# Optimization experiments

Measured on AMD Instinct MI355X. Metric: run time of the kernel, lower is better.

## Reference

```python
import jax, jax.numpy as jnp
import numpy as np

B, N, C = 8, 3136, 128
NUM_HEADS = 2
HEAD_DIM = C // NUM_HEADS  # 64
SCALE = HEAD_DIM ** -0.5


def setup_inputs() -> dict:
    key = jax.random.key(0)
    ks = jax.random.split(key, 10)
    s = 0.02
    return {
        "x": jax.random.normal(ks[0], (B, N, C), jnp.float32),
        "H": 56,
        "W": 56,
        "relative_pos": jax.random.normal(ks[1], (NUM_HEADS, N, N), jnp.float32),
        "Wq": jax.random.normal(ks[2], (C, C), jnp.float32) * s,
        "bq": jnp.zeros((C,), jnp.float32),
        "Wk": jax.random.normal(ks[3], (C, C), jnp.float32) * s,
        "bk": jnp.zeros((C,), jnp.float32),
        "Wv": jax.random.normal(ks[4], (C, C), jnp.float32) * s,
        "bv": jnp.zeros((C,), jnp.float32),
        "Wp": jax.random.normal(ks[5], (C, C), jnp.float32) * s,
        "bp": jnp.zeros((C,), jnp.float32),
    }


def reference(x, H, W, relative_pos, Wq, bq, Wk, bk, Wv, bv, Wp, bp):
    # x: [B, N, C]; sr_ratio == 1 path of Attention.forward
    b, n, c = x.shape
    h, dh = NUM_HEADS, HEAD_DIM
    # q/k/v projections -> [B, h, N, dh] (torch Linear: x @ W.T + b)
    q = (x @ Wq.T + bq).reshape(b, n, h, dh).transpose(0, 2, 1, 3)
    k = (x @ Wk.T + bk).reshape(b, n, h, dh).transpose(0, 2, 1, 3)
    v = (x @ Wv.T + bv).reshape(b, n, h, dh).transpose(0, 2, 1, 3)
    # scores with additive relative-position bias: [B, h, N, N]
    attn = jnp.einsum("bhnd,bhmd->bhnm", q, k) * SCALE + relative_pos[None]
    attn = jax.nn.softmax(attn, axis=-1)
    # AV -> [B, N, C]
    out = jnp.einsum("bhnm,bhmd->bhnd", attn, v).transpose(0, 2, 1, 3).reshape(b, n, c)
    return out @ Wp.T + bp
```

## Files before the change

### kernel.cpp

```cpp
#include <hip/hip_runtime.h>
#include <hip/hip_fp16.h>

#define N_TOK 3136
#define DH 64
#define NHEAD 2
#define CDIM 128
#define BATCH 8
#define NT 49
#define QK_SCALE 0.18033688011112f
#define LOG2E 1.4426950408889634f

typedef __attribute__((ext_vector_type(8))) short bf16x8;
typedef __attribute__((ext_vector_type(8))) _Float16 f16x8;
typedef __attribute__((ext_vector_type(2))) _Float16 f16x2;
typedef __attribute__((ext_vector_type(2))) __fp16 fp16x2;
typedef __attribute__((ext_vector_type(4))) float f32x4;
typedef __attribute__((ext_vector_type(16))) float f32x16;
typedef __attribute__((ext_vector_type(4))) unsigned short u16x4;
typedef __attribute__((ext_vector_type(4))) unsigned int u32x4;

__device__ __forceinline__ unsigned short f2bf(float f) {
  unsigned int u = __float_as_uint(f);
  u += 0x7fffu + ((u >> 16) & 1u);
  return (unsigned short)(u >> 16);
}

#define MFMA16(a, b, c)    __builtin_amdgcn_mfma_f32_16x16x32_bf16(a, b, c, 0, 0, 0)
#define MFMA32_BF(a, b, c) __builtin_amdgcn_mfma_f32_32x32x16_bf16(a, b, c, 0, 0, 0)
#define MFMA32_F16(a, b, c) __builtin_amdgcn_mfma_f32_32x32x16_f16(a, b, c, 0, 0, 0)

__device__ __forceinline__ void plswap(unsigned& a, unsigned& b) {
  asm volatile("v_permlane32_swap_b32 %0, %1" : "+v"(a), "+v"(b));
}

__device__ __forceinline__ f16x2 pkrtz(float a, float b) {
  union { fp16x2 p; f16x2 h; } cv;
  cv.p = __builtin_amdgcn_cvt_pkrtz(a, b);
  return cv.h;
}

__device__ __forceinline__ float dot2acc(f16x2 pr, float acc) {
#if __has_builtin(__builtin_amdgcn_fdot2)
  union { f16x2 h; fp16x2 p; } c; c.h = pr;
  fp16x2 ones = {(__fp16)1.0f, (__fp16)1.0f};
  return __builtin_amdgcn_fdot2(c.p, ones, acc, false);
#else
  return acc + (float)pr[0] + (float)pr[1];
#endif
}

__device__ __forceinline__ void stage_w(const float* __restrict__ W,
                                        unsigned short (*wsh)[136], int tid) {
  const float4* Wv4 = (const float4*)W;
#pragma unroll
  for (int i = 0; i < 16; ++i) {
    int f = tid + i * 256;
    float4 v = Wv4[f];
    int row = f >> 5, col = (f & 31) << 2;
    u16x4 pk = { f2bf(v.x), f2bf(v.y), f2bf(v.z), f2bf(v.w) };
    *(u16x4*)&wsh[row][col] = pk;
  }
}

__device__ __forceinline__ void mfma_block(const unsigned short (*xs)[136],
                                           const unsigned short (*wsh)[136],
                                           int w, int lk, int lg, f32x4* acc) {
#pragma unroll
  for (int nf = 0; nf < 8; ++nf) acc[nf] = (f32x4){0.f, 0.f, 0.f, 0.f};
#pragma unroll
  for (int kk = 0; kk < 4; ++kk) {
    bf16x8 a = *(const bf16x8*)&xs[w * 16 + lk][kk * 32 + 8 * lg];
#pragma unroll
    for (int nf = 0; nf < 8; ++nf) {
      bf16x8 b = *(const bf16x8*)&wsh[nf * 16 + lk][kk * 32 + 8 * lg];
      acc[nf] = MFMA16(a, b, acc[nf]);
    }
  }
}

__global__ __launch_bounds__(256)
void proj_qkv(const float* __restrict__ x,
              const float* __restrict__ Wq, const float* __restrict__ bq,
              const float* __restrict__ Wk, const float* __restrict__ bk,
              const float* __restrict__ Wv, const float* __restrict__ bv,
              unsigned short* __restrict__ qo, unsigned short* __restrict__ ko,
              unsigned short* __restrict__ vo)
{
  __shared__ __align__(16) unsigned short xs[64][136];
  __shared__ __align__(16) unsigned short wsh[128][136];
  const int tid = threadIdx.x;
  const int m0 = blockIdx.x * 64;
  const int w = tid >> 6, l = tid & 63;
  const int lk = l & 15, lg = l >> 4;

  {
    const float4* Xv = (const float4*)(x + (size_t)m0 * CDIM);
#pragma unroll
    for (int i = 0; i < 8; ++i) {
      int f = tid + i * 256;
      float4 v = Xv[f];
      int row = f >> 5, col = (f & 31) << 2;
      u16x4 pk = { f2bf(v.x), f2bf(v.y), f2bf(v.z), f2bf(v.w) };
      *(u16x4*)&xs[row][col] = pk;
    }
  }
  stage_w(Wq, wsh, tid);
  __syncthreads();

  f32x4 acc[8];

  mfma_block(xs, wsh, w, lk, lg, acc);
#pragma unroll
  for (int reg = 0; reg < 4; ++reg) {
    int row = m0 + w * 16 + 4 * lg + reg;
    int bb = row / N_TOK, tok = row - bb * N_TOK;
#pragma unroll
    for (int nf = 0; nf < 8; ++nf) {
      int col = nf * 16 + lk;
      float val = (acc[nf][reg] + bq[col]) * QK_SCALE;
      qo[((size_t)(bb * NHEAD + (nf >> 2)) * N_TOK + tok) * DH + (col & 63)] = f2bf(val);
    }
  }
  __syncthreads();

  stage_w(Wk, wsh, tid);
  __syncthreads();
  mfma_block(xs, wsh, w, lk, lg, acc);
#pragma unroll
  for (int reg = 0; reg < 4; ++reg) {
    int row = m0 + w * 16 + 4 * lg + reg;
    int bb = row / N_TOK, tok = row - bb * N_TOK;
#pragma unroll
    for (int nf = 0; nf < 8; ++nf) {
      int col = nf * 16 + lk;
      float val = acc[nf][reg] + bk[col];
      ko[((size_t)(bb * NHEAD + (nf >> 2)) * N_TOK + tok) * DH + (col & 63)] = f2bf(val);
    }
  }
  __syncthreads();

  stage_w(Wv, wsh, tid);
  __syncthreads();
  mfma_block(xs, wsh, w, lk, lg, acc);
#pragma unroll
  for (int reg = 0; reg < 4; ++reg) {
    int row = m0 + w * 16 + 4 * lg + reg;
    int bb = row / N_TOK, tok = row - bb * N_TOK;
#pragma unroll
    for (int nf = 0; nf < 8; ++nf) {
      int col = nf * 16 + lk;
      float val = acc[nf][reg] + bv[col];
      size_t idx = ((size_t)(bb * NHEAD + (nf >> 2)) * DH + (col & 63)) * N_TOK + tok;
      vo[idx] = __half_as_ushort(__float2half(val));
    }
  }
}

__global__ __launch_bounds__(256)
void exp_rp(const float* __restrict__ rp, __half* __restrict__ E)
{
  const int hkt = blockIdx.x;
  const int h = hkt / NT, kt = hkt % NT;
  const int q0 = blockIdx.y * 64;
  const int t = threadIdx.x;
  const int kp = t & 63;
  const int qi = t >> 6;

  const int ct = kp >> 5;
  const int kpp = kp & 31;
  const int hi = (kpp >> 2) & 1;
  const int r = (kpp & 3) + ((kpp >> 3) << 2);
  const int didx = hi * 32 + ct * 16 + r;

  const float* src = rp + ((size_t)h * N_TOK + q0) * N_TOK + kt * 64 + kp;
  __half* dst = E + (((size_t)h * NT + kt) * N_TOK + q0) * 64 + didx;

#pragma unroll
  for (int i = 0; i < 16; ++i) {
    int q = qi * 16 + i;
    float v = __expf(src[(size_t)q * N_TOK]);
    dst[(size_t)q * 64] = __float2half(v);
  }
}

__global__ __launch_bounds__(256)
void attn32(const unsigned short* __restrict__ q_ws,
            const unsigned short* __restrict__ k_ws,
            const unsigned short* __restrict__ v_ws,
            const __half* __restrict__ E,
            unsigned short* __restrict__ attn_out)
{
  __shared__ __align__(16) unsigned short LDSU[2][9216];

  const int b = blockIdx.x, qt = blockIdx.y, head = blockIdx.z;
  const int tid = threadIdx.x;
  const int w = tid >> 6, l = tid & 63;
  const int lq = l & 31, hi = l >> 5;

  const size_t bh = ((size_t)b * NHEAD + head) * N_TOK;
  const unsigned short* Kp = k_ws + bh * DH;
  const _Float16* Vt = (const _Float16*)v_ws + bh * DH;

  int qg = qt * 128 + w * 32 + lq;
  if (qg > N_TOK - 1) qg = N_TOK - 1;

  bf16x8 qf[4];
  {
    const unsigned short* qrow = q_ws + (bh + (size_t)qg) * DH + 8 * hi;
#pragma unroll
    for (int ks = 0; ks < 4; ++ks) qf[ks] = *(const bf16x8*)(qrow + 16 * ks);
  }

  const int kr0 = tid >> 3, ku = tid & 7;
  const int kofs = kr0 * 72 + ku * 8;
  const int gk0 = kr0 * DH + ku * 8, gk1 = gk0 + 32 * DH;
  const int gvt0 = kr0 * N_TOK + ku * 8, gvt1 = gvt0 + 32 * N_TOK;

  const __half* Eb = E + (((size_t)head * NT) * N_TOK + (size_t)qg) * DH + hi * 32;

  float lsum = 0.f;
  f32x16 o0, o1;
#pragma unroll
  for (int i = 0; i < 16; ++i) { o0[i] = 0.f; o1[i] = 0.f; }

  bf16x8 kpreA = *(const bf16x8*)(Kp + gk0);
  bf16x8 kpreB = *(const bf16x8*)(Kp + gk1);
  f16x8 vpreA = *(const f16x8*)(Vt + gvt0);
  f16x8 vpreB = *(const f16x8*)(Vt + gvt1);

  u32x4 EwA[4], EwB[4];
  {
    const u32x4* ep = (const u32x4*)Eb;
#pragma unroll
    for (int f = 0; f < 4; ++f) EwA[f] = ep[f];
  }

  *(bf16x8*)&LDSU[0][kofs] = kpreA;
  *(bf16x8*)&LDSU[0][kofs + 32 * 72] = kpreB;
  *(f16x8*)&LDSU[0][4608 + kofs] = vpreA;
  *(f16x8*)&LDSU[0][4608 + kofs + 32 * 72] = vpreB;
  {
    const unsigned short* kn = Kp + (size_t)64 * DH;
    const _Float16* vn = Vt + 64;
    kpreA = *(const bf16x8*)(kn + gk0);
    kpreB = *(const bf16x8*)(kn + gk1);
    vpreA = *(const f16x8*)(vn + gvt0);
    vpreB = *(const f16x8*)(vn + gvt1);
  }
  asm volatile("s_waitcnt lgkmcnt(0)" ::: "memory");
  __builtin_amdgcn_s_barrier();
  asm volatile("" ::: "memory");

#define ATTN_BODY(PH, KT, EW_CUR, EW_NXT, LAST)                               \
  {                                                                           \
    const unsigned short* Kb = &LDSU[PH][0];                                  \
    const unsigned short* Vb = &LDSU[PH][4608];                               \
    unsigned short* Kn = &LDSU[PH ^ 1][0];                                    \
    unsigned short* Vn = &LDSU[PH ^ 1][4608];                                 \
    if (!(LAST)) {                                         \
      const u32x4* ep = (const u32x4*)(Eb + (size_t)((KT) + 1) * (N_TOK * DH)); \
      _Pragma("unroll") for (int f = 0; f < 4; ++f) EW_NXT[f] = ep[f];        \
    }                                                                         \
                                                           \
    f32x16 s0, s1;                                                            \
    _Pragma("unroll") for (int i = 0; i < 16; ++i) { s0[i] = 0.f; s1[i] = 0.f; } \
    __builtin_amdgcn_s_setprio(1);                                            \
    _Pragma("unroll") for (int ks = 0; ks < 4; ++ks) {                        \
      bf16x8 kf0 = *(const bf16x8*)&Kb[lq * 72 + 16 * ks + 8 * hi];           \
      s0 = MFMA32_BF(kf0, qf[ks], s0);                                        \
      bf16x8 kf1 = *(const bf16x8*)&Kb[(32 + lq) * 72 + 16 * ks + 8 * hi];    \
      s1 = MFMA32_BF(kf1, qf[ks], s1);                                        \
    }                                                                         \
    __builtin_amdgcn_s_setprio(0);                                            \
    if (!(LAST)) {            \
      *(bf16x8*)&Kn[kofs] = kpreA;                                            \
      *(bf16x8*)&Kn[kofs + 32 * 72] = kpreB;                                  \
      *(f16x8*)&Vn[kofs] = vpreA;                                             \
      *(f16x8*)&Vn[kofs + 32 * 72] = vpreB;                                   \
      if ((KT) + 2 < NT) {                                                    \
        const unsigned short* kn2 = Kp + (size_t)((KT) + 2) * 64 * DH;        \
        const _Float16* vn2 = Vt + (size_t)((KT) + 2) * 64;                   \
        kpreA = *(const bf16x8*)(kn2 + gk0);                                  \
        kpreB = *(const bf16x8*)(kn2 + gk1);                                  \
        vpreA = *(const f16x8*)(vn2 + gvt0);                                  \
        vpreB = *(const f16x8*)(vn2 + gvt1);                                  \
      }                                                                       \
    }                                                                         \
                                \
    unsigned pw[16];                                                          \
    _Pragma("unroll") for (int f = 0; f < 4; ++f) {                           \
      int rb = (f & 1) * 8;                                                   \
      _Pragma("unroll") for (int i = 0; i < 4; ++i) {                         \
        float a = (f >> 1) ? s1[rb + 2 * i] : s0[rb + 2 * i];                 \
        float c = (f >> 1) ? s1[rb + 2 * i + 1] : s0[rb + 2 * i + 1];         \
        f16x2 pp = pkrtz(__builtin_amdgcn_exp2f(a), __builtin_amdgcn_exp2f(c)); \
        union { unsigned u; f16x2 h; } ec; ec.u = EW_CUR[f][i];               \
        f16x2 pr = pp * ec.h;                                                 \
        lsum = dot2acc(pr, lsum);                                             \
        union { f16x2 h; unsigned u; } pu; pu.h = pr;                         \
        pw[4 * f + i] = pu.u;                                                 \
      }                                                                       \
      plswap(pw[4 * f + 0], pw[4 * f + 2]);                                   \
      plswap(pw[4 * f + 1], pw[4 * f + 3]);                                   \
    }                                                                         \
                                                        \
    __builtin_amdgcn_s_setprio(1);                                            \
    _Pragma("unroll") for (int ks = 0; ks < 4; ++ks) {                        \
      union { unsigned u[4]; f16x8 v; } pf;                                   \
      _Pragma("unroll") for (int i = 0; i < 4; ++i) pf.u[i] = pw[4 * ks + i]; \
      f16x8 vf0 = *(const f16x8*)&Vb[lq * 72 + 16 * ks + 8 * hi];             \
      o0 = MFMA32_F16(vf0, pf.v, o0);                                         \
      f16x8 vf1 = *(const f16x8*)&Vb[(32 + lq) * 72 + 16 * ks + 8 * hi];      \
      o1 = MFMA32_F16(vf1, pf.v, o1);                                         \
    }                                                                         \
    __builtin_amdgcn_s_setprio(0);                                            \
    if (!(LAST)) {                                                            \
      asm volatile("s_waitcnt lgkmcnt(0)" ::: "memory");                      \
      __builtin_amdgcn_s_barrier();                                           \
      asm volatile("" ::: "memory");                                          \
    }                                                                         \
  }

  for (int kt2 = 0; kt2 < (NT - 1) / 2; ++kt2) {
    int kt = 2 * kt2;
    ATTN_BODY(0, kt, EwA, EwB, false);
    ATTN_BODY(1, kt + 1, EwB, EwA, false);
  }
  ATTN_BODY(0, NT - 1, EwA, EwB, true);
#undef ATTN_BODY

  lsum += __shfl_xor(lsum, 32, 64);
  float inv = 1.f / lsum;

  __syncthreads();
  unsigned short* Ot = &LDSU[0][0];
  const int orow = (w * 32 + lq) * 72;
#pragma unroll
  for (int dt = 0; dt < 2; ++dt) {
#pragma unroll
    for (int j = 0; j < 8; ++j) {
      float v0 = (dt ? o1[2 * j] : o0[2 * j]) * inv;
      float v1 = (dt ? o1[2 * j + 1] : o0[2 * j + 1]) * inv;
      unsigned pk;
      asm("v_cvt_pk_bf16_f32 %0, %1, %2" : "=v"(pk) : "v"(v0), "v"(v1));
      int d = ((2 * j) & 3) + 8 * ((2 * j) >> 2) + 4 * hi + 32 * dt;
      *(unsigned*)&Ot[orow + d] = pk;
    }
  }
  __syncthreads();
#pragma unroll
  for (int i = 0; i < 4; ++i) {
    int c = tid + 256 * i;
    int ql = c >> 3, du = c & 7;
    int tok = qt * 128 + ql;
    if (tok < N_TOK) {
      u32x4 val = *(const u32x4*)&Ot[ql * 72 + du * 8];
      *(u32x4*)&attn_out[((size_t)b * N_TOK + tok) * CDIM + head * DH + du * 8] = val;
    }
  }
}

template<bool IN_F32, int OMODE>
__global__ __launch_bounds__(256)
void proj_gemm(const void* __restrict__ Ain, const float* __restrict__ W,
               const float* __restrict__ bias, void* __restrict__ Out,
               float out_scale)
{
  __shared__ __align__(16) unsigned short xs[64][136];
  __shared__ __align__(16) unsigned short wsh[128][136];
  const int tid = threadIdx.x;
  const int m0 = blockIdx.x * 64;
  const int w = tid >> 6, l = tid & 63;
  const int lk = l & 15, lg = l >> 4;

  stage_w(W, wsh, tid);
  if (IN_F32) {
    const float4* Xv = (const float4*)((const float*)Ain + (size_t)m0 * CDIM);
#pragma unroll
    for (int i = 0; i < 8; ++i) {
      int f = tid + i * 256;
      float4 v = Xv[f];
      int row = f >> 5, col = (f & 31) << 2;
      u16x4 pk = { f2bf(v.x), f2bf(v.y), f2bf(v.z), f2bf(v.w) };
      *(u16x4*)&xs[row][col] = pk;
    }
  } else {
    const bf16x8* Xv = (const bf16x8*)((const unsigned short*)Ain + (size_t)m0 * CDIM);
#pragma unroll
    for (int i = 0; i < 4; ++i) {
      int c = tid + i * 256;
      bf16x8 v = Xv[c];
      int row = c >> 4, col = (c & 15) << 3;
      *(bf16x8*)&xs[row][col] = v;
    }
  }
  __syncthreads();

  f32x4 acc[8];
  mfma_block(xs, wsh, w, lk, lg, acc);

#pragma unroll
  for (int reg = 0; reg < 4; ++reg) {
    int row = m0 + w * 16 + 4 * lg + reg;
    int bb = row / N_TOK;
    int tok = row - bb * N_TOK;
#pragma unroll
    for (int nf = 0; nf < 8; ++nf) {
      int col = nf * 16 + lk;
      float val = (acc[nf][reg] + bias[col]) * out_scale;
      if (OMODE == 0) {
        ((float*)Out)[(size_t)row * CDIM + col] = val;
      } else {
        int head = nf >> 2;
        int d = col & 63;
        size_t idx = ((size_t)(bb * NHEAD + head) * N_TOK + tok) * DH + d;
        ((unsigned short*)Out)[idx] = f2bf(val);
      }
    }
  }
}

__global__ __launch_bounds__(256)
void attn_fallback(const unsigned short* __restrict__ q_ws,
                   const unsigned short* __restrict__ k_ws,
                   const unsigned short* __restrict__ v_ws,
                   const float* __restrict__ relpos,
                   unsigned short* __restrict__ attn_out)
{
  __shared__ __align__(16) unsigned short Ks[64][72];
  __shared__ __align__(16) unsigned short Vts[64][72];
  __shared__ __align__(16) unsigned short Ps[4][16][72];

  const int b = blockIdx.x, qt = blockIdx.y, head = blockIdx.z;
  const int tid = threadIdx.x;
  const int w = tid >> 6, l = tid & 63;
  const int lk = l & 15, lg = l >> 4;

  const size_t bh = ((size_t)b * NHEAD + head) * N_TOK;
  const unsigned short* Qp = q_ws + (bh + (size_t)qt * 64) * DH;
  const unsigned short* Kp = k_ws + bh * DH;
  const unsigned short* Vg = v_ws + bh * DH;

  bf16x8 qf0, qf1;
  {
    const unsigned short* qrow = Qp + (size_t)(w * 16 + lk) * DH + 8 * lg;
    qf0 = *(const bf16x8*)qrow;
    qf1 = *(const bf16x8*)(qrow + 32);
  }

  const int kr0 = tid >> 3;
  const int ku = (tid & 7) << 3;
  const int gk0 = kr0 * DH + ku;
  const int gk1 = gk0 + 32 * DH;
  const int vkey = tid & 63;
  const int vd0 = (tid >> 6) << 3;
  const int gv0 = vkey * DH + vd0;
  const int gv1 = gv0 + 32;

  const int qrow0 = qt * 64 + w * 16;
  const float* rpb = relpos + (size_t)head * N_TOK * N_TOK +
                     (size_t)(qrow0 + 4 * lg) * N_TOK + lk;

  float l_run[4] = {0.f, 0.f, 0.f, 0.f};
  f32x4 acc[4];
#pragma unroll
  for (int nf = 0; nf < 4; ++nf) acc[nf] = (f32x4){0.f, 0.f, 0.f, 0.f};

  bf16x8 kpreA = *(const bf16x8*)(Kp + gk0);
  bf16x8 kpreB = *(const bf16x8*)(Kp + gk1);
  bf16x8 vpreA = *(const bf16x8*)(Vg + gv0);
  bf16x8 vpreB = *(const bf16x8*)(Vg + gv1);

  for (int kt = 0; kt < NT; ++kt) {
    float rp[4][4];
#pragma unroll
    for (int r = 0; r < 4; ++r)
#pragma unroll
      for (int ct = 0; ct < 4; ++ct)
        rp[ct][r] = rpb[(size_t)r * N_TOK + kt * 64 + ct * 16];

    asm volatile("s_waitcnt lgkmcnt(0)" ::: "memory");
    __builtin_amdgcn_s_barrier();
    asm volatile("" ::: "memory");

    *(bf16x8*)&Ks[kr0][ku] = kpreA;
    *(bf16x8*)&Ks[kr0 + 32][ku] = kpreB;
#pragma unroll
    for (int j = 0; j < 8; ++j) Vts[vd0 + j][vkey] = ((const unsigned short*)&vpreA)[j];
#pragma unroll
    for (int j = 0; j < 8; ++j) Vts[vd0 + 32 + j][vkey] = ((const unsigned short*)&vpreB)[j];

    if (kt + 1 < NT) {
      const unsigned short* kn = Kp + (size_t)(kt + 1) * 64 * DH;
      const unsigned short* vn = Vg + (size_t)(kt + 1) * 64 * DH;
      kpreA = *(const bf16x8*)(kn + gk0);
      kpreB = *(const bf16x8*)(kn + gk1);
      vpreA = *(const bf16x8*)(vn + gv0);
      vpreB = *(const bf16x8*)(vn + gv1);
    }

    asm volatile("s_waitcnt lgkmcnt(0)" ::: "memory");
    __builtin_amdgcn_s_barrier();
    asm volatile("" ::: "memory");

    f32x4 s[4];
#pragma unroll
    for (int ct = 0; ct < 4; ++ct) s[ct] = (f32x4){0.f, 0.f, 0.f, 0.f};
#pragma unroll
    for (int ct = 0; ct < 4; ++ct) {
      bf16x8 kb0 = *(const bf16x8*)&Ks[ct * 16 + lk][8 * lg];
      s[ct] = MFMA16(qf0, kb0, s[ct]);
      bf16x8 kb1 = *(const bf16x8*)&Ks[ct * 16 + lk][32 + 8 * lg];
      s[ct] = MFMA16(qf1, kb1, s[ct]);
    }

#pragma unroll
    for (int ct = 0; ct < 4; ++ct) {
      float p0 = __builtin_amdgcn_exp2f(fmaf(rp[ct][0], LOG2E, s[ct][0]));
      float p1 = __builtin_amdgcn_exp2f(fmaf(rp[ct][1], LOG2E, s[ct][1]));
      float p2 = __builtin_amdgcn_exp2f(fmaf(rp[ct][2], LOG2E, s[ct][2]));
      float p3 = __builtin_amdgcn_exp2f(fmaf(rp[ct][3], LOG2E, s[ct][3]));
      l_run[0] += p0; l_run[1] += p1; l_run[2] += p2; l_run[3] += p3;
      Ps[w][4 * lg + 0][ct * 16 + lk] = f2bf(p0);
      Ps[w][4 * lg + 1][ct * 16 + lk] = f2bf(p1);
      Ps[w][4 * lg + 2][ct * 16 + lk] = f2bf(p2);
      Ps[w][4 * lg + 3][ct * 16 + lk] = f2bf(p3);
    }

    bf16x8 pa0 = *(const bf16x8*)&Ps[w][lk][8 * lg];
    bf16x8 pa1 = *(const bf16x8*)&Ps[w][lk][32 + 8 * lg];
#pragma unroll
    for (int nf = 0; nf < 4; ++nf) {
      bf16x8 vb0 = *(const bf16x8*)&Vts[nf * 16 + lk][8 * lg];
      acc[nf] = MFMA16(pa0, vb0, acc[nf]);
      bf16x8 vb1 = *(const bf16x8*)&Vts[nf * 16 + lk][32 + 8 * lg];
      acc[nf] = MFMA16(pa1, vb1, acc[nf]);
    }
  }

#pragma unroll
  for (int m = 1; m <= 8; m <<= 1)
#pragma unroll
    for (int r = 0; r < 4; ++r)
      l_run[r] += __shfl_xor(l_run[r], m, 64);

#pragma unroll
  for (int r = 0; r < 4; ++r) {
    int tok = qrow0 + 4 * lg + r;
    float inv = 1.f / l_run[r];
#pragma unroll
    for (int nf = 0; nf < 4; ++nf) {
      attn_out[((size_t)b * N_TOK + tok) * CDIM + head * DH + nf * 16 + lk] =
          f2bf(acc[nf][r] * inv);
    }
  }
}

extern "C" void kernel_launch(void* const* d_in, const int* in_sizes, int n_in,
                              void* d_out, int out_size, void* d_ws, size_t ws_size,
                              hipStream_t stream) {
  (void)in_sizes; (void)n_in; (void)out_size;
  const float* x      = (const float*)d_in[0];
  const float* relpos = (const float*)d_in[3];
  const float* Wq = (const float*)d_in[4];  const float* bq = (const float*)d_in[5];
  const float* Wk = (const float*)d_in[6];  const float* bk = (const float*)d_in[7];
  const float* Wv = (const float*)d_in[8];  const float* bv = (const float*)d_in[9];
  const float* Wp = (const float*)d_in[10]; const float* bp = (const float*)d_in[11];

  const size_t QKV_ELEMS = (size_t)BATCH * NHEAD * N_TOK * DH;
  const size_t E_ELEMS   = (size_t)NHEAD * NT * N_TOK * DH;
  unsigned short* q_ws  = (unsigned short*)d_ws;
  unsigned short* k_ws  = q_ws + QKV_ELEMS;
  unsigned short* v_ws  = k_ws + QKV_ELEMS;
  unsigned short* ao_ws = v_ws + QKV_ELEMS;
  __half* E_ws = (__half*)(ao_ws + QKV_ELEMS);

  const bool big = ws_size >= (4 * QKV_ELEMS + E_ELEMS) * sizeof(unsigned short);

  dim3 blk(256);
  const int MTILES = (BATCH * N_TOK) / 64;

  if (big) {
    proj_qkv<<<MTILES, blk, 0, stream>>>(x, Wq, bq, Wk, bk, Wv, bv, q_ws, k_ws, v_ws);
    exp_rp<<<dim3(NHEAD * NT, N_TOK / 64), blk, 0, stream>>>(relpos, E_ws);
    attn32<<<dim3(BATCH, (N_TOK + 127) / 128, NHEAD), blk, 0, stream>>>(
        q_ws, k_ws, v_ws, E_ws, ao_ws);
  } else {
    proj_gemm<true, 1><<<MTILES, blk, 0, stream>>>((const void*)x, Wq, bq, (void*)q_ws, QK_SCALE);
    proj_gemm<true, 1><<<MTILES, blk, 0, stream>>>((const void*)x, Wk, bk, (void*)k_ws, 1.f);
    proj_gemm<true, 1><<<MTILES, blk, 0, stream>>>((const void*)x, Wv, bv, (void*)v_ws, 1.f);
    attn_fallback<<<dim3(BATCH, N_TOK / 64, NHEAD), blk, 0, stream>>>(
        q_ws, k_ws, v_ws, relpos, ao_ws);
  }

  proj_gemm<false, 0><<<MTILES, blk, 0, stream>>>((const void*)ao_ws, Wp, bp, d_out, 1.f);
}
```

Measured before the change: 120.9 us.

## Split attention key range in two with combine kernel; merge projection and exp kernels

The attention kernel can now process half of the key tiles per block, which doubles the grid so more CUs stay busy. A new combine kernel sums the fp32 partial outputs and row sums, then normalizes. The QKV projection and exp(relative_pos) precompute are merged into one launch to save a launch and let the two run concurrently. The cost is extra global traffic for the partials and an additional kernel, and the path is taken only when the workspace is large enough.

New measurement: 123.1 us. No clear change (+1.8%).

```diff
diff --git a/kernel.cpp b/kernel.cpp
--- a/kernel.cpp
+++ b/kernel.cpp
@@ -7,6 +7,10 @@
 #define CDIM 128
 #define BATCH 8
 #define NT 49
+#define QTILES 25
+#define NPB (BATCH * QTILES * NHEAD)
+#define MTILES ((BATCH * N_TOK) / 64)
+#define EXPBLKS (NHEAD * NT * (N_TOK / 64))
 #define QK_SCALE 0.18033688011112f
 #define LOG2E 1.4426950408889634f
 
@@ -79,16 +83,43 @@
 }
 
 __global__ __launch_bounds__(256)
-void proj_qkv(const float* __restrict__ x,
-              const float* __restrict__ Wq, const float* __restrict__ bq,
-              const float* __restrict__ Wk, const float* __restrict__ bk,
-              const float* __restrict__ Wv, const float* __restrict__ bv,
-              unsigned short* __restrict__ qo, unsigned short* __restrict__ ko,
-              unsigned short* __restrict__ vo)
+void pre_kernel(const float* __restrict__ x,
+                const float* __restrict__ Wq, const float* __restrict__ bq,
+                const float* __restrict__ Wk, const float* __restrict__ bk,
+                const float* __restrict__ Wv, const float* __restrict__ bv,
+                unsigned short* __restrict__ qo, unsigned short* __restrict__ ko,
+                unsigned short* __restrict__ vo,
+                const float* __restrict__ rp, __half* __restrict__ E)
 {
   __shared__ __align__(16) unsigned short xs[64][136];
   __shared__ __align__(16) unsigned short wsh[128][136];
   const int tid = threadIdx.x;
+
+  if (blockIdx.x >= MTILES) {
+    const int eb = blockIdx.x - MTILES;
+    const int hkt = eb % (NHEAD * NT);
+    const int q0 = (eb / (NHEAD * NT)) * 64;
+    const int h = hkt / NT, kt = hkt % NT;
+    const int kp = tid & 63;
+    const int qi = tid >> 6;
+
+    const int ct = kp >> 5;
+    const int kpp = kp & 31;
+    const int hi = (kpp >> 2) & 1;
+    const int r = (kpp & 3) + ((kpp >> 3) << 2);
+    const int didx = hi * 32 + ct * 16 + r;
+
+    const float* src = rp + ((size_t)h * N_TOK + q0) * N_TOK + kt * 64 + kp;
+    __half* dst = E + (((size_t)h * NT + kt) * N_TOK + q0) * 64 + didx;
+#pragma unroll
+    for (int i = 0; i < 16; ++i) {
+      int q = qi * 16 + i;
+      float v = __expf(src[(size_t)q * N_TOK]);
+      dst[(size_t)q * 64] = __float2half(v);
+    }
+    return;
+  }
+
   const int m0 = blockIdx.x * 64;
   const int w = tid >> 6, l = tid & 63;
   const int lk = l & 15, lg = l >> 4;
@@ -157,42 +188,22 @@
 }
 
 __global__ __launch_bounds__(256)
-void exp_rp(const float* __restrict__ rp, __half* __restrict__ E)
-{
-  const int hkt = blockIdx.x;
-  const int h = hkt / NT, kt = hkt % NT;
-  const int q0 = blockIdx.y * 64;
-  const int t = threadIdx.x;
-  const int kp = t & 63;
-  const int qi = t >> 6;
-
-  const int ct = kp >> 5;
-  const int kpp = kp & 31;
-  const int hi = (kpp >> 2) & 1;
-  const int r = (kpp & 3) + ((kpp >> 3) << 2);
-  const int didx = hi * 32 + ct * 16 + r;
-
-  const float* src = rp + ((size_t)h * N_TOK + q0) * N_TOK + kt * 64 + kp;
-  __half* dst = E + (((size_t)h * NT + kt) * N_TOK + q0) * 64 + didx;
-
-#pragma unroll
-  for (int i = 0; i < 16; ++i) {
-    int q = qi * 16 + i;
-    float v = __expf(src[(size_t)q * N_TOK]);
-    dst[(size_t)q * 64] = __float2half(v);
-  }
-}
-
-__global__ __launch_bounds__(256)
 void attn32(const unsigned short* __restrict__ q_ws,
             const unsigned short* __restrict__ k_ws,
             const unsigned short* __restrict__ v_ws,
             const __half* __restrict__ E,
-            unsigned short* __restrict__ attn_out)
+            unsigned short* __restrict__ attn_out,
+            float* __restrict__ Opart, float* __restrict__ Lpart,
+            int split)
 {
   __shared__ __align__(16) unsigned short LDSU[2][9216];
 
-  const int b = blockIdx.x, qt = blockIdx.y, head = blockIdx.z;
+  const int b = blockIdx.x, qt = blockIdx.y;
+  const int head = split ? ((int)blockIdx.z % NHEAD) : (int)blockIdx.z;
+  const int half = split ? ((int)blockIdx.z / NHEAD) : 0;
+  const int t0   = (half == 0) ? 0 : 24;
+  const int kend = (half == 0) ? (split ? 24 : NT) : NT;
+
   const int tid = threadIdx.x;
   const int w = tid >> 6, l = tid & 63;
   const int lq = l & 31, hi = l >> 5;
@@ -223,14 +234,14 @@
 #pragma unroll
   for (int i = 0; i < 16; ++i) { o0[i] = 0.f; o1[i] = 0.f; }
 
-  bf16x8 kpreA = *(const bf16x8*)(Kp + gk0);
-  bf16x8 kpreB = *(const bf16x8*)(Kp + gk1);
-  f16x8 vpreA = *(const f16x8*)(Vt + gvt0);
-  f16x8 vpreB = *(const f16x8*)(Vt + gvt1);
+  bf16x8 kpreA = *(const bf16x8*)(Kp + (size_t)t0 * 64 * DH + gk0);
+  bf16x8 kpreB = *(const bf16x8*)(Kp + (size_t)t0 * 64 * DH + gk1);
+  f16x8 vpreA = *(const f16x8*)(Vt + (size_t)t0 * 64 + gvt0);
+  f16x8 vpreB = *(const f16x8*)(Vt + (size_t)t0 * 64 + gvt1);
 
   u32x4 EwA[4], EwB[4];
   {
-    const u32x4* ep = (const u32x4*)Eb;
+    const u32x4* ep = (const u32x4*)(Eb + (size_t)t0 * (N_TOK * DH));
 #pragma unroll
     for (int f = 0; f < 4; ++f) EwA[f] = ep[f];
   }
@@ -240,8 +251,8 @@
   *(f16x8*)&LDSU[0][4608 + kofs] = vpreA;
   *(f16x8*)&LDSU[0][4608 + kofs + 32 * 72] = vpreB;
   {
-    const unsigned short* kn = Kp + (size_t)64 * DH;
-    const _Float16* vn = Vt + 64;
+    const unsigned short* kn = Kp + (size_t)(t0 + 1) * 64 * DH;
+    const _Float16* vn = Vt + (size_t)(t0 + 1) * 64;
     kpreA = *(const bf16x8*)(kn + gk0);
     kpreB = *(const bf16x8*)(kn + gk1);
     vpreA = *(const f16x8*)(vn + gvt0);
@@ -251,17 +262,17 @@
   __builtin_amdgcn_s_barrier();
   asm volatile("" ::: "memory");
 
-#define ATTN_BODY(PH, KT, EW_CUR, EW_NXT, LAST)                               \
+#define ATTN_BODY(PH, KT, EW_CUR, EW_NXT)                                     \
   {                                                                           \
+    const bool hasNext = (KT) + 1 < kend;                                     \
     const unsigned short* Kb = &LDSU[PH][0];                                  \
     const unsigned short* Vb = &LDSU[PH][4608];                               \
     unsigned short* Kn = &LDSU[PH ^ 1][0];                                    \
     unsigned short* Vn = &LDSU[PH ^ 1][4608];                                 \
-    if (!(LAST)) {                                         \
+    if (hasNext) {                                         \
       const u32x4* ep = (const u32x4*)(Eb + (size_t)((KT) + 1) * (N_TOK * DH)); \
       _Pragma("unroll") for (int f = 0; f < 4; ++f) EW_NXT[f] = ep[f];        \
     }                                                                         \
-                                                           \
     f32x16 s0, s1;                                                            \
     _Pragma("unroll") for (int i = 0; i < 16; ++i) { s0[i] = 0.f; s1[i] = 0.f; } \
     __builtin_amdgcn_s_setprio(1);                                            \
@@ -272,12 +283,12 @@
       s1 = MFMA32_BF(kf1, qf[ks], s1);                                        \
     }                                                                         \
     __builtin_amdgcn_s_setprio(0);                                            \
-    if (!(LAST)) {            \
+    if (hasNext) {                                                            \
       *(bf16x8*)&Kn[kofs] = kpreA;                                            \
       *(bf16x8*)&Kn[kofs + 32 * 72] = kpreB;                                  \
       *(f16x8*)&Vn[kofs] = vpreA;                                             \
       *(f16x8*)&Vn[kofs + 32 * 72] = vpreB;                                   \
-      if ((KT) + 2 < NT) {                                                    \
+      if ((KT) + 2 < kend) {                                                  \
         const unsigned short* kn2 = Kp + (size_t)((KT) + 2) * 64 * DH;        \
         const _Float16* vn2 = Vt + (size_t)((KT) + 2) * 64;                   \
         kpreA = *(const bf16x8*)(kn2 + gk0);                                  \
@@ -286,7 +297,6 @@
         vpreB = *(const f16x8*)(vn2 + gvt1);                                  \
       }                                                                       \
     }                                                                         \
-                                \
     unsigned pw[16];                                                          \
     _Pragma("unroll") for (int f = 0; f < 4; ++f) {                           \
       int rb = (f & 1) * 8;                                                   \
@@ -303,7 +313,6 @@
       plswap(pw[4 * f + 0], pw[4 * f + 2]);                                   \
       plswap(pw[4 * f + 1], pw[4 * f + 3]);                                   \
     }                                                                         \
-                                                        \
     __builtin_amdgcn_s_setprio(1);                                            \
     _Pragma("unroll") for (int ks = 0; ks < 4; ++ks) {                        \
       union { unsigned u[4]; f16x8 v; } pf;                                   \
@@ -314,26 +323,103 @@
       o1 = MFMA32_F16(vf1, pf.v, o1);                                         \
     }                                                                         \
     __builtin_amdgcn_s_setprio(0);                                            \
-    if (!(LAST)) {                                                            \
+    if (hasNext) {                                                            \
       asm volatile("s_waitcnt lgkmcnt(0)" ::: "memory");                      \
       __builtin_amdgcn_s_barrier();                                           \
       asm volatile("" ::: "memory");                                          \
     }                                                                         \
   }
 
-  for (int kt2 = 0; kt2 < (NT - 1) / 2; ++kt2) {
-    int kt = 2 * kt2;
-    ATTN_BODY(0, kt, EwA, EwB, false);
-    ATTN_BODY(1, kt + 1, EwB, EwA, false);
-  }
-  ATTN_BODY(0, NT - 1, EwA, EwB, true);
+  int kt = t0;
+  while (kt + 2 <= kend) {
+    ATTN_BODY(0, kt, EwA, EwB);
+    ATTN_BODY(1, kt + 1, EwB, EwA);
+    kt += 2;
+  }
+  if (kt < kend) { ATTN_BODY(0, kt, EwA, EwB); }
 #undef ATTN_BODY
+
+  if (split) {
+    const int pb = (b * QTILES + qt) * NHEAD + head;
+    float* Op = Opart + (size_t)(half * NPB + pb) * 8192;
+#pragma unroll
+    for (int j = 0; j < 4; ++j) {
+      f32x4 v = { o0[4 * j], o0[4 * j + 1], o0[4 * j + 2], o0[4 * j + 3] };
+      *(f32x4*)&Op[(size_t)(j * 256 + tid) * 4] = v;
+    }
+#pragma unroll
+    for (int j = 0; j < 4; ++j) {
+      f32x4 v = { o1[4 * j], o1[4 * j + 1], o1[4 * j + 2], o1[4 * j + 3] };
+      *(f32x4*)&Op[(size_t)((j + 4) * 256 + tid) * 4] = v;
+    }
+    Lpart[(size_t)(half * NPB + pb) * 256 + tid] = lsum;
+    return;
+  }
 
   lsum += __shfl_xor(lsum, 32, 64);
   float inv = 1.f / lsum;
 
   __syncthreads();
   unsigned short* Ot = &LDSU[0][0];
+  const int orow = (w * 32 + lq) * 72;
+#pragma unroll
+  for (int dt = 0; dt < 2; ++dt) {
+#pragma unroll
+    for (int j = 0; j < 8; ++j) {
+      float v0 = (dt ? o1[2 * j] : o0[2 * j]) * inv;
+      float v1 = (dt ? o1[2 * j + 1] : o0[2 * j + 1]) * inv;
+      unsigned pk;
+      asm("v_cvt_pk_bf16_f32 %0, %1, %2" : "=v"(pk) : "v"(v0), "v"(v1));
+      int d = ((2 * j) & 3) + 8 * ((2 * j) >> 2) + 4 * hi + 32 * dt;
+      *(unsigned*)&Ot[orow + d] = pk;
+    }
+  }
+  __syncthreads();
+#pragma unroll
+  for (int i = 0; i < 4; ++i) {
+    int c = tid + 256 * i;
+    int ql = c >> 3, du = c & 7;
+    int tok = qt * 128 + ql;
+    if (tok < N_TOK) {
+      u32x4 val = *(const u32x4*)&Ot[ql * 72 + du * 8];
+      *(u32x4*)&attn_out[((size_t)b * N_TOK + tok) * CDIM + head * DH + du * 8] = val;
+    }
+  }
+}
+
+__global__ __launch_bounds__(256)
+void combine(const float* __restrict__ Opart, const float* __restrict__ Lpart,
+             unsigned short* __restrict__ attn_out)
+{
+  __shared__ __align__(16) unsigned short Ot[128 * 72];
+  const int b = blockIdx.x, qt = blockIdx.y, head = blockIdx.z;
+  const int tid = threadIdx.x;
+  const int w = tid >> 6, l = tid & 63;
+  const int lq = l & 31, hi = l >> 5;
+
+  const int pb = (b * QTILES + qt) * NHEAD + head;
+  const float* OpA = Opart + (size_t)pb * 8192;
+  const float* OpB = Opart + (size_t)(NPB + pb) * 8192;
+
+  f32x16 o0, o1;
+#pragma unroll
+  for (int j = 0; j < 4; ++j) {
+    f32x4 a = *(const f32x4*)&OpA[(size_t)(j * 256 + tid) * 4];
+    f32x4 c = *(const f32x4*)&OpB[(size_t)(j * 256 + tid) * 4];
+#pragma unroll
+    for (int e = 0; e < 4; ++e) o0[4 * j + e] = a[e] + c[e];
+  }
+#pragma unroll
+  for (int j = 0; j < 4; ++j) {
+    f32x4 a = *(const f32x4*)&OpA[(size_t)((j + 4) * 256 + tid) * 4];
+    f32x4 c = *(const f32x4*)&OpB[(size_t)((j + 4) * 256 + tid) * 4];
+#pragma unroll
+    for (int e = 0; e < 4; ++e) o1[4 * j + e] = a[e] + c[e];
+  }
+  float lsum = Lpart[(size_t)pb * 256 + tid] + Lpart[(size_t)(NPB + pb) * 256 + tid];
+  lsum += __shfl_xor(lsum, 32, 64);
+  float inv = 1.f / lsum;
+
   const int orow = (w * 32 + lq) * 72;
 #pragma unroll
   for (int dt = 0; dt < 2; ++dt) {
@@ -569,22 +655,33 @@
 
   const size_t QKV_ELEMS = (size_t)BATCH * NHEAD * N_TOK * DH;
   const size_t E_ELEMS   = (size_t)NHEAD * NT * N_TOK * DH;
+  const size_t OP_ELEMS  = (size_t)2 * NPB * 8192;
+  const size_t LP_ELEMS  = (size_t)2 * NPB * 256;
+
   unsigned short* q_ws  = (unsigned short*)d_ws;
   unsigned short* k_ws  = q_ws + QKV_ELEMS;
   unsigned short* v_ws  = k_ws + QKV_ELEMS;
   unsigned short* ao_ws = v_ws + QKV_ELEMS;
   __half* E_ws = (__half*)(ao_ws + QKV_ELEMS);
-
-  const bool big = ws_size >= (4 * QKV_ELEMS + E_ELEMS) * sizeof(unsigned short);
+  float* Opart = (float*)(E_ws + E_ELEMS);
+  float* Lpart = Opart + OP_ELEMS;
+
+  const size_t need_mid   = (4 * QKV_ELEMS + E_ELEMS) * sizeof(unsigned short);
+  const size_t need_split = need_mid + (OP_ELEMS + LP_ELEMS) * sizeof(float);
 
   dim3 blk(256);
-  const int MTILES = (BATCH * N_TOK) / 64;
-
-  if (big) {
-    proj_qkv<<<MTILES, blk, 0, stream>>>(x, Wq, bq, Wk, bk, Wv, bv, q_ws, k_ws, v_ws);
-    exp_rp<<<dim3(NHEAD * NT, N_TOK / 64), blk, 0, stream>>>(relpos, E_ws);
-    attn32<<<dim3(BATCH, (N_TOK + 127) / 128, NHEAD), blk, 0, stream>>>(
-        q_ws, k_ws, v_ws, E_ws, ao_ws);
+
+  if (ws_size >= need_split) {
+    pre_kernel<<<MTILES + EXPBLKS, blk, 0, stream>>>(
+        x, Wq, bq, Wk, bk, Wv, bv, q_ws, k_ws, v_ws, relpos, (__half*)E_ws);
+    attn32<<<dim3(BATCH, QTILES, NHEAD * 2), blk, 0, stream>>>(
+        q_ws, k_ws, v_ws, (const __half*)E_ws, ao_ws, Opart, Lpart, 1);
+    combine<<<dim3(BATCH, QTILES, NHEAD), blk, 0, stream>>>(Opart, Lpart, ao_ws);
+  } else if (ws_size >= need_mid) {
+    pre_kernel<<<MTILES + EXPBLKS, blk, 0, stream>>>(
+        x, Wq, bq, Wk, bk, Wv, bv, q_ws, k_ws, v_ws, relpos, (__half*)E_ws);
+    attn32<<<dim3(BATCH, QTILES, NHEAD), blk, 0, stream>>>(
+        q_ws, k_ws, v_ws, (const __half*)E_ws, ao_ws, Opart, Lpart, 0);
   } else {
     proj_gemm<true, 1><<<MTILES, blk, 0, stream>>>((const void*)x, Wq, bq, (void*)q_ws, QK_SCALE);
     proj_gemm<true, 1><<<MTILES, blk, 0, stream>>>((const void*)x, Wk, bk, (void*)k_ws, 1.f);
```

## Process two query tiles per warp in attention and merge exp/projection kernels

Applied to the files above, without the earlier changes.

Each attention warp now handles 64 queries (two 32-row groups) instead of 32, so every K/V fragment read from LDS feeds twice as many MFMAs. The grid shrinks from 25 to 13 query tiles per batch-head. The relative-position exp precompute is folded into the QKV projection launch as extra blocks, removing one kernel launch. The cost is roughly double the accumulator registers per thread, which may lower occupancy, and a smaller grid of 208 blocks that may leave compute units idle.

Measured after the change: 116.2 us. -3.9%, faster.

```diff
diff --git a/kernel.cpp b/kernel.cpp
--- a/kernel.cpp
+++ b/kernel.cpp
@@ -7,6 +7,9 @@
 #define CDIM 128
 #define BATCH 8
 #define NT 49
+#define QT2 13
+#define MTILES ((BATCH * N_TOK) / 64)
+#define EXPBLKS (NHEAD * NT * (N_TOK / 64))
 #define QK_SCALE 0.18033688011112f
 #define LOG2E 1.4426950408889634f
 
@@ -79,16 +82,43 @@
 }
 
 __global__ __launch_bounds__(256)
-void proj_qkv(const float* __restrict__ x,
-              const float* __restrict__ Wq, const float* __restrict__ bq,
-              const float* __restrict__ Wk, const float* __restrict__ bk,
-              const float* __restrict__ Wv, const float* __restrict__ bv,
-              unsigned short* __restrict__ qo, unsigned short* __restrict__ ko,
-              unsigned short* __restrict__ vo)
+void pre_kernel(const float* __restrict__ x,
+                const float* __restrict__ Wq, const float* __restrict__ bq,
+                const float* __restrict__ Wk, const float* __restrict__ bk,
+                const float* __restrict__ Wv, const float* __restrict__ bv,
+                unsigned short* __restrict__ qo, unsigned short* __restrict__ ko,
+                unsigned short* __restrict__ vo,
+                const float* __restrict__ rp, __half* __restrict__ E)
 {
   __shared__ __align__(16) unsigned short xs[64][136];
   __shared__ __align__(16) unsigned short wsh[128][136];
   const int tid = threadIdx.x;
+
+  if (blockIdx.x >= MTILES) {
+    const int eb = blockIdx.x - MTILES;
+    const int hkt = eb % (NHEAD * NT);
+    const int q0 = (eb / (NHEAD * NT)) * 64;
+    const int h = hkt / NT, kt = hkt % NT;
+    const int kp = tid & 63;
+    const int qi = tid >> 6;
+
+    const int ct = kp >> 5;
+    const int kpp = kp & 31;
+    const int hi = (kpp >> 2) & 1;
+    const int r = (kpp & 3) + ((kpp >> 3) << 2);
+    const int didx = hi * 32 + ct * 16 + r;
+
+    const float* src = rp + ((size_t)h * N_TOK + q0) * N_TOK + kt * 64 + kp;
+    __half* dst = E + (((size_t)h * NT + kt) * N_TOK + q0) * 64 + didx;
+#pragma unroll
+    for (int i = 0; i < 16; ++i) {
+      int q = qi * 16 + i;
+      float v = __expf(src[(size_t)q * N_TOK]);
+      dst[(size_t)q * 64] = __float2half(v);
+    }
+    return;
+  }
+
   const int m0 = blockIdx.x * 64;
   const int w = tid >> 6, l = tid & 63;
   const int lk = l & 15, lg = l >> 4;
@@ -153,33 +183,6 @@
       size_t idx = ((size_t)(bb * NHEAD + (nf >> 2)) * DH + (col & 63)) * N_TOK + tok;
       vo[idx] = __half_as_ushort(__float2half(val));
     }
-  }
-}
-
-__global__ __launch_bounds__(256)
-void exp_rp(const float* __restrict__ rp, __half* __restrict__ E)
-{
-  const int hkt = blockIdx.x;
-  const int h = hkt / NT, kt = hkt % NT;
-  const int q0 = blockIdx.y * 64;
-  const int t = threadIdx.x;
-  const int kp = t & 63;
-  const int qi = t >> 6;
-
-  const int ct = kp >> 5;
-  const int kpp = kp & 31;
-  const int hi = (kpp >> 2) & 1;
-  const int r = (kpp & 3) + ((kpp >> 3) << 2);
-  const int didx = hi * 32 + ct * 16 + r;
-
-  const float* src = rp + ((size_t)h * N_TOK + q0) * N_TOK + kt * 64 + kp;
-  __half* dst = E + (((size_t)h * NT + kt) * N_TOK + q0) * 64 + didx;
-
-#pragma unroll
-  for (int i = 0; i < 16; ++i) {
-    int q = qi * 16 + i;
-    float v = __expf(src[(size_t)q * N_TOK]);
-    dst[(size_t)q * 64] = __float2half(v);
   }
 }
 
@@ -201,14 +204,19 @@
   const unsigned short* Kp = k_ws + bh * DH;
   const _Float16* Vt = (const _Float16*)v_ws + bh * DH;
 
-  int qg = qt * 128 + w * 32 + lq;
-  if (qg > N_TOK - 1) qg = N_TOK - 1;
-
-  bf16x8 qf[4];
+  const int qg0 = qt * 256 + w * 64 + lq;
+  const int qgA = (qg0 < N_TOK) ? qg0 : (N_TOK - 1);
+  const int qgB = (qg0 + 32 < N_TOK) ? (qg0 + 32) : (N_TOK - 1);
+
+  bf16x8 qfA[4], qfB[4];
   {
-    const unsigned short* qrow = q_ws + (bh + (size_t)qg) * DH + 8 * hi;
-#pragma unroll
-    for (int ks = 0; ks < 4; ++ks) qf[ks] = *(const bf16x8*)(qrow + 16 * ks);
+    const unsigned short* qa = q_ws + (bh + (size_t)qgA) * DH + 8 * hi;
+    const unsigned short* qb = q_ws + (bh + (size_t)qgB) * DH + 8 * hi;
+#pragma unroll
+    for (int ks = 0; ks < 4; ++ks) {
+      qfA[ks] = *(const bf16x8*)(qa + 16 * ks);
+      qfB[ks] = *(const bf16x8*)(qb + 16 * ks);
+    }
   }
 
   const int kr0 = tid >> 3, ku = tid & 7;
@@ -216,12 +224,13 @@
   const int gk0 = kr0 * DH + ku * 8, gk1 = gk0 + 32 * DH;
   const int gvt0 = kr0 * N_TOK + ku * 8, gvt1 = gvt0 + 32 * N_TOK;
 
-  const __half* Eb = E + (((size_t)head * NT) * N_TOK + (size_t)qg) * DH + hi * 32;
-
-  float lsum = 0.f;
-  f32x16 o0, o1;
-#pragma unroll
-  for (int i = 0; i < 16; ++i) { o0[i] = 0.f; o1[i] = 0.f; }
+  const __half* EbA = E + (((size_t)head * NT) * N_TOK + (size_t)qgA) * DH + hi * 32;
+  const __half* EbB = E + (((size_t)head * NT) * N_TOK + (size_t)qgB) * DH + hi * 32;
+
+  float lsumA = 0.f, lsumB = 0.f;
+  f32x16 o0A, o1A, o0B, o1B;
+#pragma unroll
+  for (int i = 0; i < 16; ++i) { o0A[i] = 0.f; o1A[i] = 0.f; o0B[i] = 0.f; o1B[i] = 0.f; }
 
   bf16x8 kpreA = *(const bf16x8*)(Kp + gk0);
   bf16x8 kpreB = *(const bf16x8*)(Kp + gk1);
@@ -230,9 +239,10 @@
 
   u32x4 EwA[4], EwB[4];
   {
-    const u32x4* ep = (const u32x4*)Eb;
-#pragma unroll
-    for (int f = 0; f < 4; ++f) EwA[f] = ep[f];
+    const u32x4* ea = (const u32x4*)EbA;
+    const u32x4* eb = (const u32x4*)EbB;
+#pragma unroll
+    for (int f = 0; f < 4; ++f) { EwA[f] = ea[f]; EwB[f] = eb[f]; }
   }
 
   *(bf16x8*)&LDSU[0][kofs] = kpreA;
@@ -251,28 +261,51 @@
   __builtin_amdgcn_s_barrier();
   asm volatile("" ::: "memory");
 
-#define ATTN_BODY(PH, KT, EW_CUR, EW_NXT, LAST)                               \
+#define SOFTMAX(S0, S1, EW, PW, LSUM, EBASE, KT)                              \
   {                                                                           \
+    _Pragma("unroll") for (int f = 0; f < 4; ++f) {                           \
+      int rb = (f & 1) * 8;                                                   \
+      _Pragma("unroll") for (int i = 0; i < 4; ++i) {                         \
+        float a = (f >> 1) ? S1[rb + 2 * i] : S0[rb + 2 * i];                 \
+        float c = (f >> 1) ? S1[rb + 2 * i + 1] : S0[rb + 2 * i + 1];         \
+        f16x2 pp = pkrtz(__builtin_amdgcn_exp2f(a), __builtin_amdgcn_exp2f(c)); \
+        union { unsigned u; f16x2 h; } ec; ec.u = EW[f][i];                   \
+        f16x2 pr = pp * ec.h;                                                 \
+        LSUM = dot2acc(pr, LSUM);                                             \
+        union { f16x2 h; unsigned u; } pu; pu.h = pr;                         \
+        PW[4 * f + i] = pu.u;                                                 \
+      }                                                                       \
+      plswap(PW[4 * f + 0], PW[4 * f + 2]);                                   \
+      plswap(PW[4 * f + 1], PW[4 * f + 3]);                                   \
+    }                                                                         \
+    if ((KT) + 1 < NT) {           \
+      const u32x4* ep = (const u32x4*)(EBASE + (size_t)((KT) + 1) * (N_TOK * DH)); \
+      _Pragma("unroll") for (int f = 0; f < 4; ++f) EW[f] = ep[f];            \
+    }                                                                         \
+  }
+
+#define ATTN_BODY(PH, KT)                                                     \
+  {                                                                           \
+    const bool hasNext = (KT) + 1 < NT;                                       \
     const unsigned short* Kb = &LDSU[PH][0];                                  \
     const unsigned short* Vb = &LDSU[PH][4608];                               \
     unsigned short* Kn = &LDSU[PH ^ 1][0];                                    \
     unsigned short* Vn = &LDSU[PH ^ 1][4608];                                 \
-    if (!(LAST)) {                                         \
-      const u32x4* ep = (const u32x4*)(Eb + (size_t)((KT) + 1) * (N_TOK * DH)); \
-      _Pragma("unroll") for (int f = 0; f < 4; ++f) EW_NXT[f] = ep[f];        \
-    }                                                                         \
-                                                           \
-    f32x16 s0, s1;                                                            \
-    _Pragma("unroll") for (int i = 0; i < 16; ++i) { s0[i] = 0.f; s1[i] = 0.f; } \
+                                 \
+    f32x16 s0A, s1A, s0B, s1B;                                                \
+    _Pragma("unroll") for (int i = 0; i < 16; ++i)                            \
+      { s0A[i] = 0.f; s1A[i] = 0.f; s0B[i] = 0.f; s1B[i] = 0.f; }             \
     __builtin_amdgcn_s_setprio(1);                                            \
     _Pragma("unroll") for (int ks = 0; ks < 4; ++ks) {                        \
       bf16x8 kf0 = *(const bf16x8*)&Kb[lq * 72 + 16 * ks + 8 * hi];           \
-      s0 = MFMA32_BF(kf0, qf[ks], s0);                                        \
       bf16x8 kf1 = *(const bf16x8*)&Kb[(32 + lq) * 72 + 16 * ks + 8 * hi];    \
-      s1 = MFMA32_BF(kf1, qf[ks], s1);                                        \
+      s0A = MFMA32_BF(kf0, qfA[ks], s0A);                                     \
+      s0B = MFMA32_BF(kf0, qfB[ks], s0B);                                     \
+      s1A = MFMA32_BF(kf1, qfA[ks], s1A);                                     \
+      s1B = MFMA32_BF(kf1, qfB[ks], s1B);                                     \
     }                                                                         \
     __builtin_amdgcn_s_setprio(0);                                            \
-    if (!(LAST)) {            \
+    if (hasNext) {            \
       *(bf16x8*)&Kn[kofs] = kpreA;                                            \
       *(bf16x8*)&Kn[kofs + 32 * 72] = kpreB;                                  \
       *(f16x8*)&Vn[kofs] = vpreA;                                             \
@@ -286,35 +319,24 @@
         vpreB = *(const f16x8*)(vn2 + gvt1);                                  \
       }                                                                       \
     }                                                                         \
-                                \
-    unsigned pw[16];                                                          \
-    _Pragma("unroll") for (int f = 0; f < 4; ++f) {                           \
-      int rb = (f & 1) * 8;                                                   \
-      _Pragma("unroll") for (int i = 0; i < 4; ++i) {                         \
-        float a = (f >> 1) ? s1[rb + 2 * i] : s0[rb + 2 * i];                 \
-        float c = (f >> 1) ? s1[rb + 2 * i + 1] : s0[rb + 2 * i + 1];         \
-        f16x2 pp = pkrtz(__builtin_amdgcn_exp2f(a), __builtin_amdgcn_exp2f(c)); \
-        union { unsigned u; f16x2 h; } ec; ec.u = EW_CUR[f][i];               \
-        f16x2 pr = pp * ec.h;                                                 \
-        lsum = dot2acc(pr, lsum);                                             \
-        union { f16x2 h; unsigned u; } pu; pu.h = pr;                         \
-        pw[4 * f + i] = pu.u;                                                 \
-      }                                                                       \
-      plswap(pw[4 * f + 0], pw[4 * f + 2]);                                   \
-      plswap(pw[4 * f + 1], pw[4 * f + 3]);                                   \
-    }                                                                         \
-                                                        \
+    unsigned pwA[16], pwB[16];                                                \
+    SOFTMAX(s0A, s1A, EwA, pwA, lsumA, EbA, KT)                               \
+    SOFTMAX(s0B, s1B, EwB, pwB, lsumB, EbB, KT)                               \
+                              \
     __builtin_amdgcn_s_setprio(1);                                            \
     _Pragma("unroll") for (int ks = 0; ks < 4; ++ks) {                        \
-      union { unsigned u[4]; f16x8 v; } pf;                                   \
-      _Pragma("unroll") for (int i = 0; i < 4; ++i) pf.u[i] = pw[4 * ks + i]; \
+      union { unsigned u[4]; f16x8 v; } pfA, pfB;                             \
+      _Pragma("unroll") for (int i = 0; i < 4; ++i)                           \
+        { pfA.u[i] = pwA[4 * ks + i]; pfB.u[i] = pwB[4 * ks + i]; }           \
       f16x8 vf0 = *(const f16x8*)&Vb[lq * 72 + 16 * ks + 8 * hi];             \
-      o0 = MFMA32_F16(vf0, pf.v, o0);                                         \
       f16x8 vf1 = *(const f16x8*)&Vb[(32 + lq) * 72 + 16 * ks + 8 * hi];      \
-      o1 = MFMA32_F16(vf1, pf.v, o1);                                         \
+      o0A = MFMA32_F16(vf0, pfA.v, o0A);                                      \
+      o0B = MFMA32_F16(vf0, pfB.v, o0B);                                      \
+      o1A = MFMA32_F16(vf1, pfA.v, o1A);                                      \
+      o1B = MFMA32_F16(vf1, pfB.v, o1B);                                      \
     }                                                                         \
     __builtin_amdgcn_s_setprio(0);                                            \
-    if (!(LAST)) {                                                            \
+    if (hasNext) {                                                            \
       asm volatile("s_waitcnt lgkmcnt(0)" ::: "memory");                      \
       __builtin_amdgcn_s_barrier();                                           \
       asm volatile("" ::: "memory");                                          \
@@ -323,36 +345,48 @@
 
   for (int kt2 = 0; kt2 < (NT - 1) / 2; ++kt2) {
     int kt = 2 * kt2;
-    ATTN_BODY(0, kt, EwA, EwB, false);
-    ATTN_BODY(1, kt + 1, EwB, EwA, false);
-  }
-  ATTN_BODY(0, NT - 1, EwA, EwB, true);
+    ATTN_BODY(0, kt);
+    ATTN_BODY(1, kt + 1);
+  }
+  ATTN_BODY(0, NT - 1);
 #undef ATTN_BODY
-
-  lsum += __shfl_xor(lsum, 32, 64);
-  float inv = 1.f / lsum;
+#undef SOFTMAX
+
+  lsumA += __shfl_xor(lsumA, 32, 64);
+  lsumB += __shfl_xor(lsumB, 32, 64);
+  float invA = 1.f / lsumA, invB = 1.f / lsumB;
 
   __syncthreads();
   unsigned short* Ot = &LDSU[0][0];
-  const int orow = (w * 32 + lq) * 72;
+  const int rowA = (w * 64 + lq) * 72;
+  const int rowB = (w * 64 + 32 + lq) * 72;
 #pragma unroll
   for (int dt = 0; dt < 2; ++dt) {
 #pragma unroll
     for (int j = 0; j < 8; ++j) {
-      float v0 = (dt ? o1[2 * j] : o0[2 * j]) * inv;
-      float v1 = (dt ? o1[2 * j + 1] : o0[2 * j + 1]) * inv;
-      unsigned pk;
-      asm("v_cvt_pk_bf16_f32 %0, %1, %2" : "=v"(pk) : "v"(v0), "v"(v1));
       int d = ((2 * j) & 3) + 8 * ((2 * j) >> 2) + 4 * hi + 32 * dt;
-      *(unsigned*)&Ot[orow + d] = pk;
-    }
-  }
-  __syncthreads();
-#pragma unroll
-  for (int i = 0; i < 4; ++i) {
+      {
+        float v0 = (dt ? o1A[2 * j] : o0A[2 * j]) * invA;
+        float v1 = (dt ? o1A[2 * j + 1] : o0A[2 * j + 1]) * invA;
+        unsigned pk;
+        asm("v_cvt_pk_bf16_f32 %0, %1, %2" : "=v"(pk) : "v"(v0), "v"(v1));
+        *(unsigned*)&Ot[rowA + d] = pk;
+      }
+      {
+        float v0 = (dt ? o1B[2 * j] : o0B[2 * j]) * invB;
+        float v1 = (dt ? o1B[2 * j + 1] : o0B[2 * j + 1]) * invB;
+        unsigned pk;
+        asm("v_cvt_pk_bf16_f32 %0, %1, %2" : "=v"(pk) : "v"(v0), "v"(v1));
+        *(unsigned*)&Ot[rowB + d] = pk;
+      }
+    }
+  }
+  __syncthreads();
+#pragma unroll
+  for (int i = 0; i < 8; ++i) {
     int c = tid + 256 * i;
     int ql = c >> 3, du = c & 7;
-    int tok = qt * 128 + ql;
+    int tok = qt * 256 + ql;
     if (tok < N_TOK) {
       u32x4 val = *(const u32x4*)&Ot[ql * 72 + du * 8];
       *(u32x4*)&attn_out[((size_t)b * N_TOK + tok) * CDIM + head * DH + du * 8] = val;
@@ -569,22 +603,22 @@
 
   const size_t QKV_ELEMS = (size_t)BATCH * NHEAD * N_TOK * DH;
   const size_t E_ELEMS   = (size_t)NHEAD * NT * N_TOK * DH;
+
   unsigned short* q_ws  = (unsigned short*)d_ws;
   unsigned short* k_ws  = q_ws + QKV_ELEMS;
   unsigned short* v_ws  = k_ws + QKV_ELEMS;
   unsigned short* ao_ws = v_ws + QKV_ELEMS;
   __half* E_ws = (__half*)(ao_ws + QKV_ELEMS);
 
-  const bool big = ws_size >= (4 * QKV_ELEMS + E_ELEMS) * sizeof(unsigned short);
+  const size_t need_mid = (4 * QKV_ELEMS + E_ELEMS) * sizeof(unsigned short);
 
   dim3 blk(256);
-  const int MTILES = (BATCH * N_TOK) / 64;
-
-  if (big) {
-    proj_qkv<<<MTILES, blk, 0, stream>>>(x, Wq, bq, Wk, bk, Wv, bv, q_ws, k_ws, v_ws);
-    exp_rp<<<dim3(NHEAD * NT, N_TOK / 64), blk, 0, stream>>>(relpos, E_ws);
-    attn32<<<dim3(BATCH, (N_TOK + 127) / 128, NHEAD), blk, 0, stream>>>(
-        q_ws, k_ws, v_ws, E_ws, ao_ws);
+
+  if (ws_size >= need_mid) {
+    pre_kernel<<<MTILES + EXPBLKS, blk, 0, stream>>>(
+        x, Wq, bq, Wk, bk, Wv, bv, q_ws, k_ws, v_ws, relpos, (__half*)E_ws);
+    attn32<<<dim3(BATCH, QT2, NHEAD), blk, 0, stream>>>(
+        q_ws, k_ws, v_ws, (const __half*)E_ws, ao_ws);
   } else {
     proj_gemm<true, 1><<<MTILES, blk, 0, stream>>>((const void*)x, Wq, bq, (void*)q_ws, QK_SCALE);
     proj_gemm<true, 1><<<MTILES, blk, 0, stream>>>((const void*)x, Wk, bk, (void*)k_ws, 1.f);
```
